# Optimization experiments

Measured on AMD Instinct MI355X. Metric: run time of the kernel, lower is better.

## Reference

```python
import jax, jax.numpy as jnp
import numpy as np

DIM = 384; KEY_DIM = 32; HEADS = 8; ATTN_RATIO = 4; RES = 14
D = ATTN_RATIO * KEY_DIM          # 128
DH = D * HEADS                    # 1024
QK = HEADS * KEY_DIM              # 256
B = 64
EPS = 1e-5
SCALE = KEY_DIM ** -0.5


def _bn(x, p):
    # inference-mode BatchNorm; p = [gamma, beta, mean, var] each [C]; channel axis = 1
    g, b, m, v = p
    shp = (1, -1) + (1,) * (x.ndim - 2)
    return (x - m.reshape(shp)) * jax.lax.rsqrt(v.reshape(shp) + EPS) * g.reshape(shp) + b.reshape(shp)


def _bn_params(k, c):
    k1, k2, k3, k4 = jax.random.split(k, 4)
    gamma = 1.0 + 0.1 * jax.random.normal(k1, (c,), dtype=jnp.float32)
    beta = 0.02 * jax.random.normal(k2, (c,), dtype=jnp.float32)
    mean = 0.1 * jax.random.normal(k3, (c,), dtype=jnp.float32)
    var = jax.random.uniform(k4, (c,), dtype=jnp.float32) + 0.5
    return jnp.stack([gamma, beta, mean, var])


def setup_inputs() -> dict:
    key = jax.random.key(0)
    ks = jax.random.split(key, 24)
    def rn(i, shape, s=0.05):
        return s * jax.random.normal(ks[i], shape, dtype=jnp.float32)
    # relative-position bias index table: offset (|dy|,|dx|) -> dy*RES+dx
    coords = np.stack(np.meshgrid(np.arange(RES), np.arange(RES), indexing='ij'), -1).reshape(-1, 2)
    off = np.abs(coords[:, None, :] - coords[None, :, :])  # [N,N,2]
    bias_idxs = jnp.asarray(off[..., 0] * RES + off[..., 1], dtype=jnp.int32)  # [N,N]
    return {
        'x': jax.random.normal(ks[0], (B, DIM, RES, RES), dtype=jnp.float32),
        'wq': rn(1, (QK, DIM)), 'bq': rn(2, (QK,)), 'bnq': _bn_params(ks[3], QK),
        'wk': rn(4, (QK, DIM)), 'bk': rn(5, (QK,)), 'bnk': _bn_params(ks[6], QK),
        'wv': rn(7, (DH, DIM)), 'bv': rn(8, (DH,)), 'bnv': _bn_params(ks[9], DH),
        'wvl': rn(10, (DH, 1, 3, 3)), 'bvl': rn(11, (DH,)), 'bnvl': _bn_params(ks[12], DH),
        'th1w': rn(13, (HEADS, HEADS), 0.2), 'th1b': rn(14, (HEADS,)),
        'th2w': rn(15, (HEADS, HEADS), 0.2), 'th2b': rn(16, (HEADS,)),
        'wp': rn(17, (DIM, DH)), 'bp': rn(18, (DIM,)), 'bnp': _bn_params(ks[19], DIM),
        'ab': rn(20, (HEADS, RES * RES), 0.1),
        'bias_idxs': bias_idxs,
    }


def reference(x, wq, bq, bnq, wk, bk, bnk, wv, bv, bnv, wvl, bvl, bnvl,
              th1w, th1b, th2w, th2b, wp, bp, bnp, ab, bias_idxs):
    Bn, C, H, W = x.shape
    N = H * W
    xf = x.reshape(Bn, C, N)
    # 1x1 conv + BN branches (channel GEMMs)
    q = _bn(jnp.einsum('oc,bcn->bon', wq, xf) + bq[None, :, None], bnq)
    k = _bn(jnp.einsum('oc,bcn->bon', wk, xf) + bk[None, :, None], bnk)
    v = _bn(jnp.einsum('oc,bcn->bon', wv, xf) + bv[None, :, None], bnv)  # [B,DH,N]
    # local value path: 3x3 depthwise conv + BN
    v_img = v.reshape(Bn, DH, H, W)
    v_local = jax.lax.conv_general_dilated(
        v_img, wvl, window_strides=(1, 1), padding='SAME',
        feature_group_count=DH, dimension_numbers=('NCHW', 'OIHW', 'NCHW'))
    v_local = _bn(v_local + bvl[None, :, None, None], bnvl)
    # attention
    qh = q.reshape(Bn, HEADS, KEY_DIM, N).transpose(0, 1, 3, 2)  # b h n d
    kh = k.reshape(Bn, HEADS, KEY_DIM, N)                        # b h d m
    vh = v.reshape(Bn, HEADS, D, N).transpose(0, 1, 3, 2)        # b h m e
    attn = jnp.einsum('bhnd,bhdm->bhnm', qh, kh) * SCALE
    attn = attn + ab[:, bias_idxs][None]                         # [1,H,N,N] positional bias
    attn = jnp.einsum('oh,bhnm->bonm', th1w, attn) + th1b[None, :, None, None]
    attn = jax.nn.softmax(attn, axis=-1)
    attn = jnp.einsum('oh,bhnm->bonm', th2w, attn) + th2b[None, :, None, None]
    out = jnp.einsum('bhnm,bhme->bhne', attn, vh)                # b h n e
    out = out.transpose(0, 1, 3, 2).reshape(Bn, DH, H, W) + v_local
    # proj: ReLU -> 1x1 conv -> BN
    out = jax.nn.relu(out)
    out = jnp.einsum('oc,bchw->bohw', wp, out) + bp[None, :, None, None]
    return _bn(out, bnp)
```

## Files before the change

kernel.cpp:

```cpp
#include <hip/hip_runtime.h>

#define B_     64
#define DIM_   384
#define RES_   14
#define N_     196
#define HEADS_ 8
#define KD_    32
#define D_     128
#define DH_    1024
#define QK_    256
#define CH_    1536
#define EPS_   1e-5f
#define SCALE_ 0.17677669529663687f

typedef unsigned short u16;
typedef unsigned int u32;
typedef short v8s __attribute__((ext_vector_type(8)));
typedef float v4f __attribute__((ext_vector_type(4)));
typedef u16  v4u __attribute__((ext_vector_type(4)));

static __device__ __forceinline__ u16 f2bf(float f) {
    unsigned int u = __builtin_bit_cast(unsigned int, f);
    u = (u + 0x7fffu + ((u >> 16) & 1u)) >> 16;
    return (u16)u;
}
static __device__ __forceinline__ float bf2f(u16 u) {
    unsigned int x = ((unsigned int)u) << 16;
    return __builtin_bit_cast(float, x);
}
static __device__ __forceinline__ u16 f2h(float f) {
    _Float16 h = (_Float16)f;
    return __builtin_bit_cast(u16, h);
}
static __device__ __forceinline__ float h2f(u16 u) {
    return (float)__builtin_bit_cast(_Float16, u);
}

#define WBI_OFF  0u
#define WPI_OFF  589824u
#define QI_OFF   983040u
#define KI_OFF   5177344u
#define VI_OFF   9371648u
#define VLOC_U16 53411840u
#define TAIL_OFF 79101952u
#define TB_OFF   98770944u
#define ABT_OFF  98782720u
#define BIASE_OFF 98785920u

template<int KSTEPS>
static __device__ __forceinline__ void gemm_direct(
    const u16* __restrict__ Ag, const u16* __restrict__ Bg,
    v4f acc[4][4], int tid)
{
    const int lane = tid & 63, w = tid >> 6;
    const int wm = (w & 1) * 64, wn = (w >> 1) * 64;
    const int quad = lane >> 4, l16 = lane & 15;
    const u16* pa = Ag + quad * 1024 + (wm + l16) * 8;
    const u16* pb = Bg + quad * 1024 + (wn + l16) * 8;
    v8s a[2][4], b[2][4];
    #pragma unroll
    for (int i = 0; i < 4; i++) {
        a[0][i] = *(const v8s*)(pa + i * 128);
        b[0][i] = *(const v8s*)(pb + i * 128);
    }
    #pragma unroll
    for (int ks = 0; ks < KSTEPS; ks++) {
        const int cur = ks & 1, nxt = cur ^ 1;
        if (ks + 1 < KSTEPS) {
            const u16* qa = pa + (size_t)(ks + 1) * 4096;
            const u16* qb = pb + (size_t)(ks + 1) * 4096;
            #pragma unroll
            for (int i = 0; i < 4; i++) {
                a[nxt][i] = *(const v8s*)(qa + i * 128);
                b[nxt][i] = *(const v8s*)(qb + i * 128);
            }
        }
        #pragma unroll
        for (int i = 0; i < 4; i++)
            #pragma unroll
            for (int j = 0; j < 4; j++)
                acc[i][j] = __builtin_amdgcn_mfma_f32_16x16x32_bf16(a[cur][i], b[cur][j], acc[i][j], 0, 0, 0);
    }
}

__global__ __launch_bounds__(256) void k_castW(
    const float* __restrict__ wq, const float* __restrict__ wk,
    const float* __restrict__ wv, const float* __restrict__ wp,
    const float* __restrict__ ab,
    const float* __restrict__ th1w, const float* __restrict__ th1b,
    const float* __restrict__ bq, const float* __restrict__ bnq,
    const float* __restrict__ bk, const float* __restrict__ bnk,
    const float* __restrict__ bv, const float* __restrict__ bnv,
    const float* __restrict__ bp, const float* __restrict__ bnp,
    const float* __restrict__ bvl, const float* __restrict__ bnvl,
    u16* __restrict__ WbI, u16* __restrict__ WpI,
    float* __restrict__ abT1, float* __restrict__ TB)
{
    int i = blockIdx.x * 256 + threadIdx.x;
    if (i < 589824) {
        int mt = i / 49152, rem = i % 49152;
        int ks = rem >> 12, r2 = rem & 4095;
        int q = r2 >> 10, row = (r2 >> 3) & 127, e = r2 & 7;
        int c = mt * 128 + row, k = ks * 32 + q * 8 + e;
        float v = (c < 256) ? wq[c * 384 + k]
                : (c < 512) ? wk[(c - 256) * 384 + k]
                            : wv[(size_t)(c - 512) * 384 + k];
        WbI[i] = f2bf(v);
    } else if (i < 983040) {
        int j = i - 589824;
        int mt = j >> 17, rem = j & 131071;
        int ks = rem >> 12, r2 = rem & 4095;
        int q = r2 >> 10, row = (r2 >> 3) & 127, e = r2 & 7;
        int p = mt * 128 + row, k = ks * 32 + q * 8 + e;
        WpI[j] = f2bf(wp[(size_t)p * 1024 + k]);
    } else if (i < 984608) {
        int j = i - 983040;
        int idx = j >> 3, o = j & 7;
        float a = th1b[o];
        #pragma unroll
        for (int h = 0; h < 8; h++) a += th1w[o * 8 + h] * ab[h * N_ + idx];
        abT1[j] = a;
    } else if (i < 987552) {
        int j = i - 984608;
        if (j < 256) {
            int c = j;
            float s = bnq[c] * rsqrtf(bnq[768 + c] + EPS_);
            float t = (bq[c] - bnq[512 + c]) * s + bnq[256 + c];
            TB[c] = s * SCALE_; TB[256 + c] = t * SCALE_;
        } else if (j < 512) {
            int c = j - 256;
            float s = bnk[c] * rsqrtf(bnk[768 + c] + EPS_);
            float t = (bk[c] - bnk[512 + c]) * s + bnk[256 + c];
            TB[512 + c] = s; TB[768 + c] = t;
        } else if (j < 1536) {
            int c = j - 512;
            float s = bnv[c] * rsqrtf(bnv[3072 + c] + EPS_);
            float t = (bv[c] - bnv[2048 + c]) * s + bnv[1024 + c];
            TB[1024 + c] = s; TB[2048 + c] = t;
        } else if (j < 1920) {
            int c = j - 1536;
            float s = bnp[c] * rsqrtf(bnp[1152 + c] + EPS_);
            float t = (bp[c] - bnp[768 + c]) * s + bnp[384 + c];
            TB[3072 + c] = s; TB[3456 + c] = t;
        } else {
            int c = j - 1920;
            float s = bnvl[c] * rsqrtf(bnvl[3072 + c] + EPS_);
            float t = (bvl[c] - bnvl[2048 + c]) * s + bnvl[1024 + c];
            TB[3840 + c] = s; TB[4864 + c] = t;
        }
    }
}

__global__ __launch_bounds__(256) void k_bias(
    const float* __restrict__ abT1, const int* __restrict__ bidx,
    float* __restrict__ biasE)
{
    int i = blockIdx.x * 256 + threadIdx.x;
    if (i >= N_ * 8 * N_) return;
    int m = i % N_;
    int t = i / N_;
    int o = t & 7;
    int n = t >> 3;
    biasE[i] = abT1[bidx[n * N_ + m] * 8 + o] - 5.f;
}

__global__ __launch_bounds__(256) void k_castX(
    const float* __restrict__ x, u16* __restrict__ xI)
{
    __shared__ float T[64][65];
    const int tid = threadIdx.x;
    const int n0 = blockIdx.x * 64;
    const int k0 = blockIdx.y * 64;
    const int b  = blockIdx.z;
    const int c = tid & 63, r4 = tid >> 6;
    #pragma unroll
    for (int i = 0; i < 16; i++) {
        int kr = i * 4 + r4;
        int gn = n0 + c;
        T[kr][c] = (gn < N_) ? x[((size_t)b * DIM_ + k0 + kr) * N_ + gn] : 0.f;
    }
    __syncthreads();
    #pragma unroll
    for (int it = 0; it < 16; it++) {
        int j = it * 256 + tid;
        int kk = j & 63, nn = j >> 6;
        int k = k0 + kk, n = n0 + nn;
        xI[(size_t)b * 98304 + (n >> 7) * 49152 + (k >> 5) * 4096
           + ((k >> 3) & 3) * 1024 + (n & 127) * 8 + (k & 7)] = f2bf(T[kk][nn]);
    }
}

__global__ __launch_bounds__(256) void k_qkv(
    const u16* __restrict__ WbI, const u16* __restrict__ xI,
    const float* __restrict__ TB,
    u16* __restrict__ qI, u16* __restrict__ kI, u16* __restrict__ vI)
{
    const int tid = threadIdx.x;
    const int L = blockIdx.x + 2 * (blockIdx.y + 12 * blockIdx.z);
    const int idx = L >> 3;
    const int b  = (L & 7) * 8 + idx / 24;
    const int r  = idx % 24;
    const int mt = r >> 1, nt = r & 1;
    v4f acc[4][4] = {};
    gemm_direct<12>(WbI + (size_t)mt * 49152,
                    xI + ((size_t)b * 2 + nt) * 49152, acc, tid);

    const int lane = tid & 63, w = tid >> 6;
    const int wm = (w & 1) * 64, wn = (w >> 1) * 64;
    const int quad = lane >> 4, l16 = lane & 15;
    #pragma unroll
    for (int i = 0; i < 4; i++) {
        #pragma unroll
        for (int j = 0; j < 4; j++) {
            int gc = mt * 128 + wm + i * 16 + quad * 4;
            int n  = nt * 128 + wn + j * 16 + l16;
            v4f v = acc[i][j];
            if (gc < 256) {
                v4f s = *(const v4f*)&TB[gc];
                v4f t = *(const v4f*)&TB[256 + gc];
                v4u u;
                #pragma unroll
                for (int r2 = 0; r2 < 4; r2++) u[r2] = f2bf(v[r2] * s[r2] + t[r2]);
                *(v4u*)&qI[((size_t)(b * 8 + (gc >> 5)) * 256 + n) * 32 + (gc & 31)] = u;
            } else if (gc < 512) {
                int c = gc - 256;
                v4f s = *(const v4f*)&TB[512 + c];
                v4f t = *(const v4f*)&TB[768 + c];
                v4u u;
                #pragma unroll
                for (int r2 = 0; r2 < 4; r2++) u[r2] = f2bf(v[r2] * s[r2] + t[r2]);
                *(v4u*)&kI[((size_t)(b * 8 + (c >> 5)) * 256 + n) * 32 + (c & 31)] = u;
            } else {
                int c = gc - 512;
                if (n < 224) {
                    int o = c >> 7, e = c & 127;
                    u16* base = vI + ((size_t)(b * 8 + o) * 7 + (n >> 5)) * 4096
                                + ((n >> 3) & 3) * 1024 + (n & 7);
                    #pragma unroll
                    for (int r2 = 0; r2 < 4; r2++) {
                        u16 outv = 0;
                        if (n < N_) outv = f2bf(v[r2] * TB[1024 + c + r2] + TB[2048 + c + r2]);
                        base[(e + r2) * 8] = outv;
                    }
                }
            }
        }
    }
}

__global__ __launch_bounds__(256) void k_dwconv(
    const u16* __restrict__ vI, const float* __restrict__ wvl,
    const float* __restrict__ TB, u16* __restrict__ vlocI)
{
    __shared__ u16 V[64 * 230];
    const int tid = threadIdx.x;
    const int sub = blockIdx.x;
    const int b   = blockIdx.y;
    const int o   = sub >> 1;
    const int e0  = (sub & 1) * 64;
    const u16* img = vI + (size_t)(b * 8 + o) * 28672;

    {
        const int quad = tid >> 6, l = tid & 63;
        #pragma unroll
        for (int i = 0; i < 7; i++) {
            v8s u = *(const v8s*)&img[i * 4096 + quad * 1024 + (e0 + l) * 8];
            const u32* ui = (const u32*)&u;
            int m0 = i * 32 + quad * 8;
            u32* dst = (u32*)&V[l * 230 + m0];
            #pragma unroll
            for (int c = 0; c < 4; c++) dst[c] = ui[c];
        }
    }
    __syncthreads();

    const int e = tid & 63, j = tid >> 6;
    const int cg = sub * 64 + e;
    const int y0 = j * 4;
    const int ny = (j == 3) ? 2 : 4;
    float wgt[9];
    #pragma unroll
    for (int k = 0; k < 9; k++) wgt[k] = wvl[cg * 9 + k];
    const float sc = TB[3840 + cg], sh = TB[4864 + cg];
    u32 po[4][7];

    for (int yi = 0; yi < ny; yi++) {
        int y = y0 + yi;
        float a[3][16];
        #pragma unroll
        for (int dy = 0; dy < 3; dy++) {
            int yy = y + dy - 1;
            a[dy][0] = 0.f; a[dy][15] = 0.f;
            if (yy < 0 || yy > 13) {
                #pragma unroll
                for (int x = 1; x < 15; x++) a[dy][x] = 0.f;
            } else {
                const u16* rp = &V[e * 230 + yy * 14];
                #pragma unroll
                for (int c4 = 0; c4 < 7; c4++) {
                    u32 u = *(const u32*)&rp[c4 * 2];
                    a[dy][1 + 2 * c4] = bf2f((u16)(u & 0xffffu));
                    a[dy][2 + 2 * c4] = bf2f((u16)(u >> 16));
                }
            }
        }
        #pragma unroll
        for (int xp = 0; xp < 7; xp++) {
            u32 pk = 0;
            #pragma unroll
            for (int half = 0; half < 2; half++) {
                int x = 2 * xp + half;
                float s = 0.f;
                #pragma unroll
                for (int dy = 0; dy < 3; dy++)
                    #pragma unroll
                    for (int kx = 0; kx < 3; kx++)
                        s += wgt[dy * 3 + kx] * a[dy][x + kx];
                u16 bv = f2bf(s * sc + sh);
                pk |= ((u32)bv) << (16 * half);
            }
            po[yi][xp] = pk;
        }
    }
    __syncthreads();

    for (int yi = 0; yi < ny; yi++) {
        u32* dst = (u32*)&V[e * 196 + (y0 + yi) * 14];
        #pragma unroll
        for (int xp = 0; xp < 7; xp++) dst[xp] = po[yi][xp];
    }
    __syncthreads();

    for (int it = 0; it < 7; it++) {
        int idx = it * 256 + tid;
        if (idx < 1568) {
            int g = idx / 196, n = idx - g * 196;
            v4u lo, hi;
            #pragma unroll
            for (int r = 0; r < 4; r++) lo[r] = V[(g * 8 + r) * 196 + n];
            #pragma unroll
            for (int r = 0; r < 4; r++) hi[r] = V[(g * 8 + 4 + r) * 196 + n];
            u16* dst = vlocI + ((size_t)(b * 2 + (n >> 7)) * 32 + sub * 2 + (g >> 2)) * 4096
                     + (g & 3) * 1024 + (n & 127) * 8;
            *(v4u*)dst = lo;
            *(v4u*)(dst + 4) = hi;
        }
    }
}

__global__ __launch_bounds__(512) void k_attn_av(
    const u16* __restrict__ qI, const u16* __restrict__ kI,
    const u16* __restrict__ vI,
    const float* __restrict__ th1w,
    const float* __restrict__ th2w, const float* __restrict__ th2b,
    const float* __restrict__ biasE,
    const u16* __restrict__ vlocI, u16* __restrict__ aoI)
{
    __shared__ u16 Sl[8 * 8 * 228];
    __shared__ float red[64][8];
    __shared__ float invS[64];
    const int tid = threadIdx.x;
    const int w = tid >> 6, lane = tid & 63;
    const int quad = lane >> 4, l16 = lane & 15;
    const int L = blockIdx.x + 25 * blockIdx.y;
    const int idx = L >> 3;
    const int b  = (L & 7) * 8 + idx / 25;
    const int qt = idx % 25;
    const int n0 = qt * 8;

    {
        const int h = w;
        const u16* qb = qI + (size_t)(b * 8 + h) * 8192;
        const u16* kb = kI + (size_t)(b * 8 + h) * 8192;
        v8s qf = *(const v8s*)&qb[(n0 + l16) * 32 + quad * 8];
        #pragma unroll
        for (int mt = 0; mt < 13; mt++) {
            v8s kf = *(const v8s*)&kb[(mt * 16 + l16) * 32 + quad * 8];
            v4f acc = {};
            acc = __builtin_amdgcn_mfma_f32_16x16x32_bf16(kf, qf, acc, 0, 0, 0);
            if (l16 < 8) {
                v4u pk;
                #pragma unroll
                for (int r = 0; r < 4; r++) pk[r] = f2h(acc[r]);
                *(v4u*)&Sl[(h * 8 + l16) * 228 + mt * 16 + quad * 4] = pk;
            }
        }
    }
    __syncthreads();

    const int mp  = (tid & 127) * 2;
    const int qh2 = tid >> 7;
    const bool pvalid = (mp < N_);
    for (int qq = 0; qq < 2; qq++) {
        int q = qh2 * 2 + qq;
        int n = n0 + q;
        if (pvalid && n < N_) {
            const float* bE = biasE + (size_t)n * 1568 + mp;
            float S0[8], S1[8];
            #pragma unroll
            for (int h = 0; h < 8; h++) {
                u32 u = *(const u32*)&Sl[(h * 8 + q) * 228 + mp];
                S0[h] = h2f((u16)(u & 0xffffu));
                S1[h] = h2f((u16)(u >> 16));
            }
            u32 ew[8];
            #pragma unroll
            for (int o = 0; o < 8; o++) {
                float2 bb = *(const float2*)&bE[o * 196];
                float a0 = bb.x, a1 = bb.y;
                #pragma unroll
                for (int h = 0; h < 8; h++) {
                    a0 += th1w[o * 8 + h] * S0[h];
                    a1 += th1w[o * 8 + h] * S1[h];
                }
                ew[o] = (u32)f2h(__expf(a0)) | ((u32)f2h(__expf(a1)) << 16);
            }
            #pragma unroll
            for (int o = 0; o < 8; o++)
                *(u32*)&Sl[(o * 8 + q) * 228 + mp] = ew[o];
        }
    }
    __syncthreads();

    {
        int r = tid >> 3, oct = tid & 7;
        int mstart = oct * 24;
        int cnt = (oct == 7) ? 14 : 12;
        const u16* rowp = &Sl[r * 228 + mstart];
        float s = 0.f;
        for (int i = 0; i < cnt; i++) {
            u32 u = *(const u32*)&rowp[i * 2];
            s += h2f((u16)(u & 0xffffu)) + h2f((u16)(u >> 16));
        }
        red[r][oct] = s;
    }
    __syncthreads();
    if (tid < 64) {
        float s = 0.f;
        #pragma unroll
        for (int i = 0; i < 8; i++) s += red[tid][i];
        invS[tid] = 1.f / s;
    }
    __syncthreads();

    for (int qq = 0; qq < 2; qq++) {
        int q = qh2 * 2 + qq;
        bool valid = pvalid && (n0 + q < N_);
        u32 pw[8];
        if (valid) {
            float s0[8], s1[8];
            #pragma unroll
            for (int h = 0; h < 8; h++) {
                u32 u = *(const u32*)&Sl[(h * 8 + q) * 228 + mp];
                float is = invS[h * 8 + q];
                s0[h] = h2f((u16)(u & 0xffffu)) * is;
                s1[h] = h2f((u16)(u >> 16)) * is;
            }
            #pragma unroll
            for (int o = 0; o < 8; o++) {
                float v0 = th2b[o], v1 = th2b[o];
                #pragma unroll
                for (int h = 0; h < 8; h++) {
                    v0 += th2w[o * 8 + h] * s0[h];
                    v1 += th2w[o * 8 + h] * s1[h];
                }
                pw[o] = (u32)f2bf(v0) | ((u32)f2bf(v1) << 16);
            }
        } else {
            #pragma unroll
            for (int o = 0; o < 8; o++) pw[o] = 0;
        }
        if (mp < 224) {
            #pragma unroll
            for (int o = 0; o < 8; o++)
                *(u32*)&Sl[(o * 8 + q) * 228 + mp] = pw[o];
        }
    }
    __syncthreads();

    {
        const int half_ = n0 >> 7;
        const int row0 = n0 & 127;
        const int n = n0 + l16;
        const bool act = (l16 < 8) && (n < N_);
        const int o = w;
        const u16* vb = vI + (size_t)(b * 8 + o) * 28672;
        const u16* prow = &Sl[(o * 8 + (l16 & 7)) * 228];
        __builtin_amdgcn_s_setprio(1);
        #pragma unroll
        for (int eh = 0; eh < 2; eh++) {
            v4f acc[4] = {};
            v8s a[2][4];
            const u16* ab0 = vb + quad * 1024 + (eh * 64 + l16) * 8;
            #pragma unroll
            for (int e = 0; e < 4; e++) a[0][e] = *(const v8s*)(ab0 + e * 128);
            #pragma unroll
            for (int ks = 0; ks < 7; ks++) {
                const int cur = ks & 1, nxt = cur ^ 1;
                if (ks < 6) {
                    const u16* an = ab0 + (size_t)(ks + 1) * 4096;
                    #pragma unroll
                    for (int e = 0; e < 4; e++) a[nxt][e] = *(const v8s*)(an + e * 128);
                }
                v8s bfr = *(const v8s*)&prow[ks * 32 + quad * 8];
                #pragma unroll
                for (int e = 0; e < 4; e++)
                    acc[e] = __builtin_amdgcn_mfma_f32_16x16x32_bf16(a[cur][e], bfr, acc[e], 0, 0, 0);
            }
            if (act) {
                #pragma unroll
                for (int e = 0; e < 4; e++) {
                    const int c0 = o * 128 + (eh * 4 + e) * 16 + quad * 4;
                    const size_t ioff = ((size_t)(b * 2 + half_) * 32 + (c0 >> 5)) * 4096
                                      + ((c0 >> 3) & 3) * 1024 + (size_t)(row0 + l16) * 8 + (c0 & 7);
                    v4u lv = *(const v4u*)&vlocI[ioff];
                    v4u u;
                    #pragma unroll
                    for (int r = 0; r < 4; r++)
                        u[r] = f2bf(fmaxf(acc[e][r] + bf2f(lv[r]), 0.f));
                    *(v4u*)&aoI[ioff] = u;
                }
            }
        }
        __builtin_amdgcn_s_setprio(0);
    }
}

__global__ __launch_bounds__(256) void k_proj(
    const u16* __restrict__ WpI, const u16* __restrict__ aoI,
    const float* __restrict__ TB, float* __restrict__ out)
{
    const int tid = threadIdx.x;
    const int L = blockIdx.x + 2 * (blockIdx.y + 3 * blockIdx.z);
    const int idx = L >> 3;
    const int b  = (L & 7) * 8 + idx / 6;
    const int r  = idx % 6;
    const int mt = r >> 1, nt = r & 1;
    v4f acc[4][4] = {};
    gemm_direct<32>(WpI + (size_t)mt * 131072,
                    aoI + ((size_t)b * 2 + nt) * 131072, acc, tid);

    const int lane = tid & 63, w = tid >> 6;
    const int wm = (w & 1) * 64, wn = (w >> 1) * 64;
    const int quad = lane >> 4, l16 = lane & 15;
    #pragma unroll
    for (int i = 0; i < 4; i++) {
        #pragma unroll
        for (int j = 0; j < 4; j++) {
            int p0 = mt * 128 + wm + i * 16 + quad * 4;
            int n  = nt * 128 + wn + j * 16 + l16;
            if (n < N_) {
                v4f s = *(const v4f*)&TB[3072 + p0];
                v4f t = *(const v4f*)&TB[3456 + p0];
                #pragma unroll
                for (int r2 = 0; r2 < 4; r2++)
                    out[((size_t)b * DIM_ + p0 + r2) * N_ + n] = acc[i][j][r2] * s[r2] + t[r2];
            }
        }
    }
}

extern "C" void kernel_launch(void* const* d_in, const int* in_sizes, int n_in,
                              void* d_out, int out_size, void* d_ws, size_t ws_size,
                              hipStream_t stream)
{
    const float* x    = (const float*)d_in[0];
    const float* wq   = (const float*)d_in[1];
    const float* bq   = (const float*)d_in[2];
    const float* bnq  = (const float*)d_in[3];
    const float* wk   = (const float*)d_in[4];
    const float* bk   = (const float*)d_in[5];
    const float* bnk  = (const float*)d_in[6];
    const float* wv   = (const float*)d_in[7];
    const float* bv   = (const float*)d_in[8];
    const float* bnv  = (const float*)d_in[9];
    const float* wvl  = (const float*)d_in[10];
    const float* bvl  = (const float*)d_in[11];
    const float* bnvl = (const float*)d_in[12];
    const float* th1w = (const float*)d_in[13];
    const float* th1b = (const float*)d_in[14];
    const float* th2w = (const float*)d_in[15];
    const float* th2b = (const float*)d_in[16];
    const float* wp   = (const float*)d_in[17];
    const float* bp   = (const float*)d_in[18];
    const float* bnp  = (const float*)d_in[19];
    const float* ab   = (const float*)d_in[20];
    const int*   bidx = (const int*)d_in[21];
    float* out = (float*)d_out;

    u16* wsb  = (u16*)d_ws;
    u16* WbI  = wsb + WBI_OFF;
    u16* WpI  = wsb + WPI_OFF;
    u16* qI   = wsb + QI_OFF;
    u16* kI   = wsb + KI_OFF;
    u16* vI   = wsb + VI_OFF;
    u16* vlocI = wsb + VLOC_U16;
    u16* xI   = wsb + TAIL_OFF;
    u16* aoI  = wsb + TAIL_OFF;
    float* TB    = (float*)(wsb + TB_OFF);
    float* abT1  = (float*)(wsb + ABT_OFF);
    float* biasE = (float*)(wsb + BIASE_OFF);

    k_castW<<<dim3(3859), 256, 0, stream>>>(wq, wk, wv, wp, ab, th1w, th1b,
                                            bq, bnq, bk, bnk, bv, bnv, bp, bnp, bvl, bnvl,
                                            WbI, WpI, abT1, TB);
    k_bias<<<dim3((N_ * 8 * N_ + 255) / 256), 256, 0, stream>>>(abT1, bidx, biasE);
    k_castX<<<dim3(4, 6, B_), 256, 0, stream>>>(x, xI);
    k_qkv<<<dim3(2, 12, B_), 256, 0, stream>>>(WbI, xI, TB, qI, kI, vI);
    k_dwconv<<<dim3(16, B_), 256, 0, stream>>>(vI, wvl, TB, vlocI);
    k_attn_av<<<dim3(25, B_), 512, 0, stream>>>(qI, kI, vI, th1w, th2w, th2b,
                                                biasE, vlocI, aoI);
    k_proj<<<dim3(2, 3, B_), 256, 0, stream>>>(WpI, aoI, TB, out);
}
```

Baseline: 268.2 us.

## Fuse preprocessing kernels, double attention query tile, deepen proj GEMM prefetch

Merges the weight cast, bias-table expansion and input transpose/cast into one launch, which removes two kernel launches and the intermediate abT1 table. The attention kernel now handles 16 queries per block instead of 8, so every MFMA tile row is used and K/V reads are amortised over twice as many queries, while the LDS footprint doubles. The projection GEMM switches to a three-stage register prefetch, which raises register pressure.

```diff
diff --git a/kernel.cpp b/kernel.cpp
--- a/kernel.cpp
+++ b/kernel.cpp
@@ -44,7 +44,6 @@
 #define VLOC_U16 53411840u
 #define TAIL_OFF 79101952u
 #define TB_OFF   98770944u
-#define ABT_OFF  98782720u
 #define BIASE_OFF 98785920u
 
 template<int KSTEPS>
@@ -83,7 +82,47 @@
     }
 }
 
-__global__ __launch_bounds__(256) void k_castW(
+template<int KSTEPS>
+static __device__ __forceinline__ void gemm_direct3(
+    const u16* __restrict__ Ag, const u16* __restrict__ Bg,
+    v4f acc[4][4], int tid)
+{
+    const int lane = tid & 63, w = tid >> 6;
+    const int wm = (w & 1) * 64, wn = (w >> 1) * 64;
+    const int quad = lane >> 4, l16 = lane & 15;
+    const u16* pa = Ag + quad * 1024 + (wm + l16) * 8;
+    const u16* pb = Bg + quad * 1024 + (wn + l16) * 8;
+    v8s a[3][4], b[3][4];
+    #pragma unroll
+    for (int s = 0; s < 2; s++) {
+        #pragma unroll
+        for (int i = 0; i < 4; i++) {
+            a[s][i] = *(const v8s*)(pa + (size_t)s * 4096 + i * 128);
+            b[s][i] = *(const v8s*)(pb + (size_t)s * 4096 + i * 128);
+        }
+    }
+    #pragma unroll
+    for (int ks = 0; ks < KSTEPS; ks++) {
+        const int cur = ks % 3, nxt = (ks + 2) % 3;
+        if (ks + 2 < KSTEPS) {
+            const u16* qa = pa + (size_t)(ks + 2) * 4096;
+            const u16* qb = pb + (size_t)(ks + 2) * 4096;
+            #pragma unroll
+            for (int i = 0; i < 4; i++) {
+                a[nxt][i] = *(const v8s*)(qa + i * 128);
+                b[nxt][i] = *(const v8s*)(qb + i * 128);
+            }
+        }
+        #pragma unroll
+        for (int i = 0; i < 4; i++)
+            #pragma unroll
+            for (int j = 0; j < 4; j++)
+                acc[i][j] = __builtin_amdgcn_mfma_f32_16x16x32_bf16(a[cur][i], b[cur][j], acc[i][j], 0, 0, 0);
+    }
+}
+
+__global__ __launch_bounds__(256) void k_pre(
+    const float* __restrict__ x,
     const float* __restrict__ wq, const float* __restrict__ wk,
     const float* __restrict__ wv, const float* __restrict__ wp,
     const float* __restrict__ ab,
@@ -93,10 +132,36 @@
     const float* __restrict__ bv, const float* __restrict__ bnv,
     const float* __restrict__ bp, const float* __restrict__ bnp,
     const float* __restrict__ bvl, const float* __restrict__ bnvl,
-    u16* __restrict__ WbI, u16* __restrict__ WpI,
-    float* __restrict__ abT1, float* __restrict__ TB)
-{
-    int i = blockIdx.x * 256 + threadIdx.x;
+    const int* __restrict__ bidx,
+    u16* __restrict__ xI, u16* __restrict__ WbI, u16* __restrict__ WpI,
+    float* __restrict__ TB, float* __restrict__ biasE)
+{
+    __shared__ float T[64][65];
+    const int tid = threadIdx.x;
+    if (blockIdx.x < 1536) {
+        const int t  = blockIdx.x;
+        const int n0 = (t & 3) * 64;
+        const int k0 = ((t >> 2) % 6) * 64;
+        const int b  = t / 24;
+        const int c = tid & 63, r4 = tid >> 6;
+        #pragma unroll
+        for (int i = 0; i < 16; i++) {
+            int kr = i * 4 + r4;
+            int gn = n0 + c;
+            T[kr][c] = (gn < N_) ? x[((size_t)b * DIM_ + k0 + kr) * N_ + gn] : 0.f;
+        }
+        __syncthreads();
+        #pragma unroll
+        for (int it = 0; it < 16; it++) {
+            int j = it * 256 + tid;
+            int kk = j & 63, nn = j >> 6;
+            int k = k0 + kk, n = n0 + nn;
+            xI[(size_t)b * 98304 + (n >> 7) * 49152 + (k >> 5) * 4096
+               + ((k >> 3) & 3) * 1024 + (n & 127) * 8 + (k & 7)] = f2bf(T[kk][nn]);
+        }
+        return;
+    }
+    int i = (blockIdx.x - 1536) * 256 + tid;
     if (i < 589824) {
         int mt = i / 49152, rem = i % 49152;
         int ks = rem >> 12, r2 = rem & 4095;
@@ -113,15 +178,8 @@
         int q = r2 >> 10, row = (r2 >> 3) & 127, e = r2 & 7;
         int p = mt * 128 + row, k = ks * 32 + q * 8 + e;
         WpI[j] = f2bf(wp[(size_t)p * 1024 + k]);
-    } else if (i < 984608) {
+    } else if (i < 985984) {
         int j = i - 983040;
-        int idx = j >> 3, o = j & 7;
-        float a = th1b[o];
-        #pragma unroll
-        for (int h = 0; h < 8; h++) a += th1w[o * 8 + h] * ab[h * N_ + idx];
-        abT1[j] = a;
-    } else if (i < 987552) {
-        int j = i - 984608;
         if (j < 256) {
             int c = j;
             float s = bnq[c] * rsqrtf(bnq[768 + c] + EPS_);
@@ -148,45 +206,17 @@
             float t = (bvl[c] - bnvl[2048 + c]) * s + bnvl[1024 + c];
             TB[3840 + c] = s; TB[4864 + c] = t;
         }
-    }
-}
-
-__global__ __launch_bounds__(256) void k_bias(
-    const float* __restrict__ abT1, const int* __restrict__ bidx,
-    float* __restrict__ biasE)
-{
-    int i = blockIdx.x * 256 + threadIdx.x;
-    if (i >= N_ * 8 * N_) return;
-    int m = i % N_;
-    int t = i / N_;
-    int o = t & 7;
-    int n = t >> 3;
-    biasE[i] = abT1[bidx[n * N_ + m] * 8 + o] - 5.f;
-}
-
-__global__ __launch_bounds__(256) void k_castX(
-    const float* __restrict__ x, u16* __restrict__ xI)
-{
-    __shared__ float T[64][65];
-    const int tid = threadIdx.x;
-    const int n0 = blockIdx.x * 64;
-    const int k0 = blockIdx.y * 64;
-    const int b  = blockIdx.z;
-    const int c = tid & 63, r4 = tid >> 6;
-    #pragma unroll
-    for (int i = 0; i < 16; i++) {
-        int kr = i * 4 + r4;
-        int gn = n0 + c;
-        T[kr][c] = (gn < N_) ? x[((size_t)b * DIM_ + k0 + kr) * N_ + gn] : 0.f;
-    }
-    __syncthreads();
-    #pragma unroll
-    for (int it = 0; it < 16; it++) {
-        int j = it * 256 + tid;
-        int kk = j & 63, nn = j >> 6;
-        int k = k0 + kk, n = n0 + nn;
-        xI[(size_t)b * 98304 + (n >> 7) * 49152 + (k >> 5) * 4096
-           + ((k >> 3) & 3) * 1024 + (n & 127) * 8 + (k & 7)] = f2bf(T[kk][nn]);
+    } else if (i < 1293312) {
+        int j = i - 985984;
+        int m = j % N_;
+        int t = j / N_;
+        int o = t & 7;
+        int n = t >> 3;
+        int idx = bidx[n * N_ + m];
+        float a = th1b[o];
+        #pragma unroll
+        for (int h = 0; h < 8; h++) a += th1w[o * 8 + h] * ab[h * N_ + idx];
+        biasE[j] = a - 5.f;
     }
 }
 
@@ -356,17 +386,17 @@
     const float* __restrict__ biasE,
     const u16* __restrict__ vlocI, u16* __restrict__ aoI)
 {
-    __shared__ u16 Sl[8 * 8 * 228];
-    __shared__ float red[64][8];
-    __shared__ float invS[64];
+    __shared__ u16 Sl[8 * 16 * 228];
+    __shared__ float red[128][4];
+    __shared__ float invS[128];
     const int tid = threadIdx.x;
     const int w = tid >> 6, lane = tid & 63;
     const int quad = lane >> 4, l16 = lane & 15;
-    const int L = blockIdx.x + 25 * blockIdx.y;
+    const int L = blockIdx.x + 13 * blockIdx.y;
     const int idx = L >> 3;
-    const int b  = (L & 7) * 8 + idx / 25;
-    const int qt = idx % 25;
-    const int n0 = qt * 8;
+    const int b  = (L & 7) * 8 + idx / 13;
+    const int qt = idx % 13;
+    const int n0 = qt * 16;
 
     {
         const int h = w;
@@ -378,28 +408,26 @@
             v8s kf = *(const v8s*)&kb[(mt * 16 + l16) * 32 + quad * 8];
             v4f acc = {};
             acc = __builtin_amdgcn_mfma_f32_16x16x32_bf16(kf, qf, acc, 0, 0, 0);
-            if (l16 < 8) {
-                v4u pk;
-                #pragma unroll
-                for (int r = 0; r < 4; r++) pk[r] = f2h(acc[r]);
-                *(v4u*)&Sl[(h * 8 + l16) * 228 + mt * 16 + quad * 4] = pk;
-            }
+            v4u pk;
+            #pragma unroll
+            for (int r = 0; r < 4; r++) pk[r] = f2h(acc[r]);
+            *(v4u*)&Sl[(h * 16 + l16) * 228 + mt * 16 + quad * 4] = pk;
         }
     }
     __syncthreads();
 
     const int mp  = (tid & 127) * 2;
-    const int qh2 = tid >> 7;
+    const int qh  = tid >> 7;
     const bool pvalid = (mp < N_);
-    for (int qq = 0; qq < 2; qq++) {
-        int q = qh2 * 2 + qq;
+    for (int qq = 0; qq < 4; qq++) {
+        int q = qh * 4 + qq;
         int n = n0 + q;
         if (pvalid && n < N_) {
             const float* bE = biasE + (size_t)n * 1568 + mp;
             float S0[8], S1[8];
             #pragma unroll
             for (int h = 0; h < 8; h++) {
-                u32 u = *(const u32*)&Sl[(h * 8 + q) * 228 + mp];
+                u32 u = *(const u32*)&Sl[(h * 16 + q) * 228 + mp];
                 S0[h] = h2f((u16)(u & 0xffffu));
                 S1[h] = h2f((u16)(u >> 16));
             }
@@ -417,42 +445,38 @@
             }
             #pragma unroll
             for (int o = 0; o < 8; o++)
-                *(u32*)&Sl[(o * 8 + q) * 228 + mp] = ew[o];
+                *(u32*)&Sl[(o * 16 + q) * 228 + mp] = ew[o];
         }
     }
     __syncthreads();
 
     {
-        int r = tid >> 3, oct = tid & 7;
-        int mstart = oct * 24;
-        int cnt = (oct == 7) ? 14 : 12;
+        int r = tid >> 2, quarter = tid & 3;
+        int mstart = quarter * 48;
+        int cnt = (quarter == 3) ? 26 : 24;
         const u16* rowp = &Sl[r * 228 + mstart];
         float s = 0.f;
         for (int i = 0; i < cnt; i++) {
             u32 u = *(const u32*)&rowp[i * 2];
             s += h2f((u16)(u & 0xffffu)) + h2f((u16)(u >> 16));
         }
-        red[r][oct] = s;
-    }
-    __syncthreads();
-    if (tid < 64) {
-        float s = 0.f;
-        #pragma unroll
-        for (int i = 0; i < 8; i++) s += red[tid][i];
-        invS[tid] = 1.f / s;
-    }
-    __syncthreads();
-
-    for (int qq = 0; qq < 2; qq++) {
-        int q = qh2 * 2 + qq;
+        red[r][quarter] = s;
+    }
+    __syncthreads();
+    if (tid < 128)
+        invS[tid] = 1.f / (red[tid][0] + red[tid][1] + red[tid][2] + red[tid][3]);
+    __syncthreads();
+
+    for (int qq = 0; qq < 4; qq++) {
+        int q = qh * 4 + qq;
         bool valid = pvalid && (n0 + q < N_);
         u32 pw[8];
         if (valid) {
             float s0[8], s1[8];
             #pragma unroll
             for (int h = 0; h < 8; h++) {
-                u32 u = *(const u32*)&Sl[(h * 8 + q) * 228 + mp];
-                float is = invS[h * 8 + q];
+                u32 u = *(const u32*)&Sl[(h * 16 + q) * 228 + mp];
+                float is = invS[h * 16 + q];
                 s0[h] = h2f((u16)(u & 0xffffu)) * is;
                 s1[h] = h2f((u16)(u >> 16)) * is;
             }
@@ -473,7 +497,7 @@
         if (mp < 224) {
             #pragma unroll
             for (int o = 0; o < 8; o++)
-                *(u32*)&Sl[(o * 8 + q) * 228 + mp] = pw[o];
+                *(u32*)&Sl[(o * 16 + q) * 228 + mp] = pw[o];
         }
     }
     __syncthreads();
@@ -482,10 +506,10 @@
         const int half_ = n0 >> 7;
         const int row0 = n0 & 127;
         const int n = n0 + l16;
-        const bool act = (l16 < 8) && (n < N_);
+        const bool act = (n < N_);
         const int o = w;
         const u16* vb = vI + (size_t)(b * 8 + o) * 28672;
-        const u16* prow = &Sl[(o * 8 + (l16 & 7)) * 228];
+        const u16* prow = &Sl[(o * 16 + l16) * 228];
         __builtin_amdgcn_s_setprio(1);
         #pragma unroll
         for (int eh = 0; eh < 2; eh++) {
@@ -537,8 +561,8 @@
     const int r  = idx % 6;
     const int mt = r >> 1, nt = r & 1;
     v4f acc[4][4] = {};
-    gemm_direct<32>(WpI + (size_t)mt * 131072,
-                    aoI + ((size_t)b * 2 + nt) * 131072, acc, tid);
+    gemm_direct3<32>(WpI + (size_t)mt * 131072,
+                     aoI + ((size_t)b * 2 + nt) * 131072, acc, tid);
 
     const int lane = tid & 63, w = tid >> 6;
     const int wm = (w & 1) * 64, wn = (w >> 1) * 64;
@@ -598,17 +622,14 @@
     u16* xI   = wsb + TAIL_OFF;
     u16* aoI  = wsb + TAIL_OFF;
     float* TB    = (float*)(wsb + TB_OFF);
-    float* abT1  = (float*)(wsb + ABT_OFF);
     float* biasE = (float*)(wsb + BIASE_OFF);
 
-    k_castW<<<dim3(3859), 256, 0, stream>>>(wq, wk, wv, wp, ab, th1w, th1b,
-                                            bq, bnq, bk, bnk, bv, bnv, bp, bnp, bvl, bnvl,
-                                            WbI, WpI, abT1, TB);
-    k_bias<<<dim3((N_ * 8 * N_ + 255) / 256), 256, 0, stream>>>(abT1, bidx, biasE);
-    k_castX<<<dim3(4, 6, B_), 256, 0, stream>>>(x, xI);
+    k_pre<<<dim3(6588), 256, 0, stream>>>(x, wq, wk, wv, wp, ab, th1w, th1b,
+                                          bq, bnq, bk, bnk, bv, bnv, bp, bnp, bvl, bnvl,
+                                          bidx, xI, WbI, WpI, TB, biasE);
     k_qkv<<<dim3(2, 12, B_), 256, 0, stream>>>(WbI, xI, TB, qI, kI, vI);
     k_dwconv<<<dim3(16, B_), 256, 0, stream>>>(vI, wvl, TB, vlocI);
-    k_attn_av<<<dim3(25, B_), 512, 0, stream>>>(qI, kI, vI, th1w, th2w, th2b,
+    k_attn_av<<<dim3(13, B_), 512, 0, stream>>>(qI, kI, vI, th1w, th2w, th2b,
                                                 biasE, vlocI, aoI);
     k_proj<<<dim3(2, 3, B_), 256, 0, stream>>>(WpI, aoI, TB, out);
 }
```

New measurement: 251.6 us. 1.07x faster.
